# Kernel optimization log

Measured on AMD Instinct MI355X. Metric: run time of the kernel, lower is better.

Reference implementation:

```python
import jax, jax.numpy as jnp
import numpy as np

POS_WEIGHT = 5.0

def setup_inputs() -> dict:
    key = jax.random.key(0)
    k1, k2, k3, k4 = jax.random.split(key, 4)
    B, S, P = 128, 32768, 65536
    preds = jax.random.normal(k1, (B, S), dtype=jnp.float32)
    targets = jax.random.randint(k2, (B, S), 0, 2, dtype=jnp.int32)
    # monotone (sorted) warping-path indices, like a DTW alignment path
    pi = jnp.sort(jax.random.randint(k3, (B, P), 0, S), axis=1)
    pj = jnp.sort(jax.random.randint(k4, (B, P), 0, S), axis=1)
    paths = jnp.stack([pi, pj], axis=-1).astype(jnp.int64)  # [B, P, 2]
    return {"preds": preds, "targets": targets, "paths": paths}

def _per_batch_loss(pred, target, path):
    # pred: [S], target: [S] int, path: [P, 2] of (i, j) pairs
    S = pred.shape[0]
    P = path.shape[0]
    pi, pj = path[:, 0], path[:, 1]
    steps = jnp.arange(P)
    # first step index k at which each target position j appears in the path
    first_k = jax.ops.segment_min(steps, pj, num_segments=S)  # [S]
    is_first = steps == first_k[pj]                            # first occurrence of j
    hit = (target[pj] == 1) & is_first                         # first-match to an SoS target
    # scatter-first-write: gt[i] = 1 for the matched pred positions
    gt = jnp.zeros((S,), dtype=pred.dtype).at[pi].max(hit.astype(pred.dtype))
    # BCEWithLogitsLoss with pos_weight, mean reduction (numerically stable)
    loss = -(POS_WEIGHT * gt * jax.nn.log_sigmoid(pred)
             + (1.0 - gt) * jax.nn.log_sigmoid(-pred))
    return loss.mean()

def reference(preds, targets, paths):
    per_batch = jax.vmap(_per_batch_loss)(preds, targets, paths)  # [B]
    return per_batch.mean()  # sum over batch / batch_size
```

## Files before the change

### kernel.cpp

```cpp
#include <hip/hip_runtime.h>

#define NB 128
#define NS 32768
#define NP 65536
#define POS_W 5.0f

constexpr int MASK_WORDS = (NB * NS) / 32;
constexpr int WPB        = NS / 32;
constexpr int LOSS_BLOCKS = 1024;


__global__ __launch_bounds__(256)
void tbit_kernel(const int* __restrict__ targets, unsigned int* __restrict__ tb) {
    constexpr int NSEG = NB * NS / 64;
    const int lane = threadIdx.x & 63;
    const int wid  = (blockIdx.x * blockDim.x + threadIdx.x) >> 6;
    const int nw   = (gridDim.x * blockDim.x) >> 6;
    for (int s = wid; s < NSEG; s += nw) {
        const unsigned long long m = __ballot(targets[(size_t)s * 64 + lane] != 0);
        if (lane == 0)       tb[s * 2]     = (unsigned int)m;
        else if (lane == 32) tb[s * 2 + 1] = (unsigned int)(m >> 32);
    }
}

template <int QPB>
__global__ __launch_bounds__(1024)
void gt_kernel(const int* __restrict__ pw, const unsigned int* __restrict__ tbits_g,
               unsigned int* __restrict__ pmask) {
    __shared__ unsigned int tbits[WPB];
    __shared__ unsigned int gbits[WPB];

    const int is64 = (pw[2 * (size_t)NP - 1] == 0);

    const int q   = blockIdx.x;
    const int b   = blockIdx.y;
    const int tid = threadIdx.x;
    const int lane = tid & 63;

    tbits[tid] = tbits_g[(size_t)b * WPB + tid];
    gbits[tid] = 0u;
    __syncthreads();

    constexpr int STEPS = NP / QPB;
    const int k0 = q * STEPS;
    const int4* p4 = (const int4*)pw;

    if (is64) {
        #pragma unroll 4
        for (int it = 0; it < STEPS / 1024; ++it) {
            const int k = k0 + it * 1024 + tid;
            const size_t step = (size_t)b * NP + (size_t)k;
            const int4 a = p4[step];
            const int pi = a.x, pj = a.z;
            const int prev = __shfl_up(pj, 1);
            bool f;
            if (lane == 0) {
                f = (k == 0) ? true : (pj != pw[((size_t)(2 * step - 1)) << 1]);
            } else {
                f = (pj != prev);
            }
            if (f && ((tbits[pj >> 5] >> (pj & 31)) & 1u)) {
                atomicOr(&gbits[pi >> 5], 1u << (pi & 31));
            }
        }
    } else {
        #pragma unroll 4
        for (int it = 0; it < STEPS / 2048; ++it) {
            const int k = k0 + (it * 1024 + tid) * 2;
            const size_t step = (size_t)b * NP + (size_t)k;
            const int4 a = p4[step >> 1];
            const int pi0 = a.x, pj0 = a.y, pi1 = a.z, pj1 = a.w;
            const int prev = __shfl_up(pj1, 1);
            bool f0;
            if (lane == 0) {
                f0 = (k == 0) ? true : (pj0 != pw[2 * step - 1]);
            } else {
                f0 = (pj0 != prev);
            }
            const bool f1 = (pj1 != pj0);
            if (f0 && ((tbits[pj0 >> 5] >> (pj0 & 31)) & 1u))
                atomicOr(&gbits[pi0 >> 5], 1u << (pi0 & 31));
            if (f1 && ((tbits[pj1 >> 5] >> (pj1 & 31)) & 1u))
                atomicOr(&gbits[pi1 >> 5], 1u << (pi1 & 31));
        }
    }
    __syncthreads();

    pmask[(size_t)q * MASK_WORDS + (size_t)b * WPB + tid] = gbits[tid];
}

__global__ __launch_bounds__(256)
void loss_kernel(const float* __restrict__ preds, const unsigned int* __restrict__ pmask,
                 float* __restrict__ partials, int qpb) {
    constexpr int N4 = (NB * NS) / 4;
    float acc = 0.f;
    const int stride = gridDim.x * blockDim.x;
    for (int idx = blockIdx.x * blockDim.x + threadIdx.x; idx < N4; idx += stride) {
        const float4 x = reinterpret_cast<const float4*>(preds)[idx];
        unsigned int mw = 0u;
        for (int q = 0; q < qpb; ++q)
            mw |= pmask[(size_t)q * MASK_WORDS + (idx >> 3)];
        const unsigned int m = mw >> ((idx & 7) * 4);
        const float xs[4] = {x.x, x.y, x.z, x.w};
#pragma unroll
        for (int j = 0; j < 4; ++j) {
            const float v = xs[j];
            const float t = __logf(1.f + __expf(-fabsf(v)));
            const float sp_pos = t + fmaxf(v, 0.f);
            const float sp_neg = sp_pos - v;
            acc += ((m >> j) & 1u) ? POS_W * sp_neg : sp_pos;
        }
    }
    for (int off = 32; off; off >>= 1) acc += __shfl_down(acc, off);
    __shared__ float sacc[4];
    const int wave = threadIdx.x >> 6, lane = threadIdx.x & 63;
    if (lane == 0) sacc[wave] = acc;
    __syncthreads();
    if (threadIdx.x == 0) {
        float s = 0.f;
#pragma unroll
        for (int w = 0; w < 4; ++w) s += sacc[w];
        partials[blockIdx.x] = s;
    }
}

__global__ __launch_bounds__(256)
void final_kernel(const float* __restrict__ partials, float* __restrict__ out) {
    float acc = 0.f;
    for (int i = threadIdx.x; i < LOSS_BLOCKS; i += 256) acc += partials[i];
    for (int off = 32; off; off >>= 1) acc += __shfl_down(acc, off);
    __shared__ float sacc[4];
    const int wave = threadIdx.x >> 6, lane = threadIdx.x & 63;
    if (lane == 0) sacc[wave] = acc;
    __syncthreads();
    if (threadIdx.x == 0) {
        float s = 0.f;
#pragma unroll
        for (int w = 0; w < 4; ++w) s += sacc[w];
        out[0] = s * (1.0f / ((float)NB * (float)NS));
    }
}

extern "C" void kernel_launch(void* const* d_in, const int* in_sizes, int n_in,
                              void* d_out, int out_size, void* d_ws, size_t ws_size,
                              hipStream_t stream) {
    const float* preds   = (const float*)d_in[0];
    const int*   targets = (const int*)d_in[1];
    const int*   paths_w = (const int*)d_in[2];
    float*       out     = (float*)d_out;

    int qpb = 4;
    while (qpb > 1 &&
           ws_size < (size_t)(1 + qpb) * MASK_WORDS * 4 + (size_t)LOSS_BLOCKS * 4)
        qpb >>= 1;

    unsigned int* tbits_g  = (unsigned int*)d_ws;
    unsigned int* pmask    = tbits_g + MASK_WORDS;
    float*        partials = (float*)((char*)d_ws +
                              (size_t)(1 + qpb) * MASK_WORDS * 4);

    tbit_kernel<<<1024, 256, 0, stream>>>(targets, tbits_g);

    dim3 g1(qpb, NB);
    switch (qpb) {
        case 4: gt_kernel<4><<<g1, 1024, 0, stream>>>(paths_w, tbits_g, pmask); break;
        case 2: gt_kernel<2><<<g1, 1024, 0, stream>>>(paths_w, tbits_g, pmask); break;
        default: gt_kernel<1><<<g1, 1024, 0, stream>>>(paths_w, tbits_g, pmask); break;
    }

    loss_kernel<<<LOSS_BLOCKS, 256, 0, stream>>>(preds, pmask, partials, qpb);
    final_kernel<<<1, 256, 0, stream>>>(partials, out);
}
```

Measured before the change: 34.09 us.

## Give each gt thread a contiguous run of path steps and split the path eight ways

gt_kernel now runs 512 threads per block, and each thread walks a contiguous chunk of path steps. Within a chunk it tracks the previous pj in a register instead of using a wavefront shuffle, and it loads 16 steps at a time to raise memory-level parallelism. The path is split across up to 8 blocks per batch, and loss_kernel is templated on the split count so its mask-OR loop unrolls. The costs are strided per-thread global loads that no longer coalesce across lanes, more partial mask words to read and OR in the loss kernel, and a larger workspace.

```diff
diff --git a/kernel.cpp b/kernel.cpp
--- a/kernel.cpp
+++ b/kernel.cpp
@@ -24,7 +24,7 @@
 }
 
 template <int QPB>
-__global__ __launch_bounds__(1024)
+__global__ __launch_bounds__(512)
 void gt_kernel(const int* __restrict__ pw, const unsigned int* __restrict__ tbits_g,
                unsigned int* __restrict__ pmask) {
     __shared__ unsigned int tbits[WPB];
@@ -35,70 +35,83 @@
     const int q   = blockIdx.x;
     const int b   = blockIdx.y;
     const int tid = threadIdx.x;
-    const int lane = tid & 63;
 
-    tbits[tid] = tbits_g[(size_t)b * WPB + tid];
-    gbits[tid] = 0u;
+    tbits[tid]       = tbits_g[(size_t)b * WPB + tid];
+    tbits[tid + 512] = tbits_g[(size_t)b * WPB + tid + 512];
+    gbits[tid]       = 0u;
+    gbits[tid + 512] = 0u;
     __syncthreads();
 
     constexpr int STEPS = NP / QPB;
-    const int k0 = q * STEPS;
-    const int4* p4 = (const int4*)pw;
+    constexpr int SPT   = STEPS / 512;
+    const int    k0 = q * STEPS + tid * SPT;
+    const size_t s0 = (size_t)b * NP + (size_t)k0;
+    const int4*  p4 = (const int4*)pw;
 
+    int prev = -1;
     if (is64) {
-        #pragma unroll 4
-        for (int it = 0; it < STEPS / 1024; ++it) {
-            const int k = k0 + it * 1024 + tid;
-            const size_t step = (size_t)b * NP + (size_t)k;
-            const int4 a = p4[step];
-            const int pi = a.x, pj = a.z;
-            const int prev = __shfl_up(pj, 1);
-            bool f;
-            if (lane == 0) {
-                f = (k == 0) ? true : (pj != pw[((size_t)(2 * step - 1)) << 1]);
-            } else {
-                f = (pj != prev);
-            }
-            if (f && ((tbits[pj >> 5] >> (pj & 31)) & 1u)) {
-                atomicOr(&gbits[pi >> 5], 1u << (pi & 31));
+        if (k0 != 0) prev = pw[4 * s0 - 2];
+        #pragma unroll
+        for (int c = 0; c < SPT / 16; ++c) {
+            const size_t base = s0 + (size_t)c * 16;
+            int4 a[16];
+            #pragma unroll
+            for (int j = 0; j < 16; ++j) a[j] = p4[base + j];
+            #pragma unroll
+            for (int j = 0; j < 16; ++j) {
+                const int pi = a[j].x, pj = a[j].z;
+                const bool f = (pj != prev);
+                prev = pj;
+                if (f && ((tbits[pj >> 5] >> (pj & 31)) & 1u))
+                    atomicOr(&gbits[pi >> 5], 1u << (pi & 31));
             }
         }
     } else {
-        #pragma unroll 4
-        for (int it = 0; it < STEPS / 2048; ++it) {
-            const int k = k0 + (it * 1024 + tid) * 2;
-            const size_t step = (size_t)b * NP + (size_t)k;
-            const int4 a = p4[step >> 1];
-            const int pi0 = a.x, pj0 = a.y, pi1 = a.z, pj1 = a.w;
-            const int prev = __shfl_up(pj1, 1);
-            bool f0;
-            if (lane == 0) {
-                f0 = (k == 0) ? true : (pj0 != pw[2 * step - 1]);
-            } else {
-                f0 = (pj0 != prev);
+        if (k0 != 0) prev = pw[2 * s0 - 1];
+        #pragma unroll
+        for (int c = 0; c < SPT / 16; ++c) {
+            const size_t base = (s0 >> 1) + (size_t)c * 8;
+            int4 a[8];
+            #pragma unroll
+            for (int j = 0; j < 8; ++j) a[j] = p4[base + j];
+            #pragma unroll
+            for (int j = 0; j < 8; ++j) {
+                {
+                    const int pi = a[j].x, pj = a[j].y;
+                    const bool f = (pj != prev);
+                    prev = pj;
+                    if (f && ((tbits[pj >> 5] >> (pj & 31)) & 1u))
+                        atomicOr(&gbits[pi >> 5], 1u << (pi & 31));
+                }
+                {
+                    const int pi = a[j].z, pj = a[j].w;
+                    const bool f = (pj != prev);
+                    prev = pj;
+                    if (f && ((tbits[pj >> 5] >> (pj & 31)) & 1u))
+                        atomicOr(&gbits[pi >> 5], 1u << (pi & 31));
+                }
             }
-            const bool f1 = (pj1 != pj0);
-            if (f0 && ((tbits[pj0 >> 5] >> (pj0 & 31)) & 1u))
-                atomicOr(&gbits[pi0 >> 5], 1u << (pi0 & 31));
-            if (f1 && ((tbits[pj1 >> 5] >> (pj1 & 31)) & 1u))
-                atomicOr(&gbits[pi1 >> 5], 1u << (pi1 & 31));
         }
     }
     __syncthreads();
 
-    pmask[(size_t)q * MASK_WORDS + (size_t)b * WPB + tid] = gbits[tid];
+    unsigned int* dst = pmask + (size_t)q * MASK_WORDS + (size_t)b * WPB;
+    dst[tid]       = gbits[tid];
+    dst[tid + 512] = gbits[tid + 512];
 }
 
+template <int QPB>
 __global__ __launch_bounds__(256)
 void loss_kernel(const float* __restrict__ preds, const unsigned int* __restrict__ pmask,
-                 float* __restrict__ partials, int qpb) {
+                 float* __restrict__ partials) {
     constexpr int N4 = (NB * NS) / 4;
     float acc = 0.f;
     const int stride = gridDim.x * blockDim.x;
     for (int idx = blockIdx.x * blockDim.x + threadIdx.x; idx < N4; idx += stride) {
         const float4 x = reinterpret_cast<const float4*>(preds)[idx];
         unsigned int mw = 0u;
-        for (int q = 0; q < qpb; ++q)
+        #pragma unroll
+        for (int q = 0; q < QPB; ++q)
             mw |= pmask[(size_t)q * MASK_WORDS + (idx >> 3)];
         const unsigned int m = mw >> ((idx & 7) * 4);
         const float xs[4] = {x.x, x.y, x.z, x.w};
@@ -149,7 +162,7 @@
     const int*   paths_w = (const int*)d_in[2];
     float*       out     = (float*)d_out;
 
-    int qpb = 4;
+    int qpb = 8;
     while (qpb > 1 &&
            ws_size < (size_t)(1 + qpb) * MASK_WORDS * 4 + (size_t)LOSS_BLOCKS * 4)
         qpb >>= 1;
@@ -163,11 +176,23 @@
 
     dim3 g1(qpb, NB);
     switch (qpb) {
-        case 4: gt_kernel<4><<<g1, 1024, 0, stream>>>(paths_w, tbits_g, pmask); break;
-        case 2: gt_kernel<2><<<g1, 1024, 0, stream>>>(paths_w, tbits_g, pmask); break;
-        default: gt_kernel<1><<<g1, 1024, 0, stream>>>(paths_w, tbits_g, pmask); break;
+        case 8:
+            gt_kernel<8><<<g1, 512, 0, stream>>>(paths_w, tbits_g, pmask);
+            loss_kernel<8><<<LOSS_BLOCKS, 256, 0, stream>>>(preds, pmask, partials);
+            break;
+        case 4:
+            gt_kernel<4><<<g1, 512, 0, stream>>>(paths_w, tbits_g, pmask);
+            loss_kernel<4><<<LOSS_BLOCKS, 256, 0, stream>>>(preds, pmask, partials);
+            break;
+        case 2:
+            gt_kernel<2><<<g1, 512, 0, stream>>>(paths_w, tbits_g, pmask);
+            loss_kernel<2><<<LOSS_BLOCKS, 256, 0, stream>>>(preds, pmask, partials);
+            break;
+        default:
+            gt_kernel<1><<<g1, 512, 0, stream>>>(paths_w, tbits_g, pmask);
+            loss_kernel<1><<<LOSS_BLOCKS, 256, 0, stream>>>(preds, pmask, partials);
+            break;
     }
 
-    loss_kernel<<<LOSS_BLOCKS, 256, 0, stream>>>(preds, pmask, partials, qpb);
     final_kernel<<<1, 256, 0, stream>>>(partials, out);
 }
```

After: 35.24 us. 3.4% more time.
